# Optimization experiments

Measured on AMD Instinct MI355X. Metric: run time of the kernel, lower is better.

## Reference

```python
import jax, jax.numpy as jnp
import numpy as np
import math

HIDDEN = 512
BATCH, SEQ = 4, 4096


def setup_inputs() -> dict:
    key = jax.random.key(0)
    ks = jax.random.split(key, 7)
    s = 1.0 / math.sqrt(HIDDEN)
    return {
        "X": jax.random.normal(ks[0], (BATCH, SEQ, HIDDEN), dtype=jnp.float32),
        "Wq": jax.random.uniform(ks[1], (HIDDEN, HIDDEN), jnp.float32, -s, s),
        "bq": jax.random.uniform(ks[2], (HIDDEN,), jnp.float32, -s, s),
        "Wk": jax.random.uniform(ks[3], (HIDDEN, HIDDEN), jnp.float32, -s, s),
        "bk": jax.random.uniform(ks[4], (HIDDEN,), jnp.float32, -s, s),
        "Wv": jax.random.uniform(ks[5], (HIDDEN, HIDDEN), jnp.float32, -s, s),
        "bv": jax.random.uniform(ks[6], (HIDDEN,), jnp.float32, -s, s),
    }


def reference(X, Wq, bq, Wk, bk, Wv, bv):
    # Q, K, V projections (torch Linear: y = x @ W.T + b; here W stored as [in, out])
    Q = jnp.einsum("bsd,de->bse", X, Wq) + bq
    K = jnp.einsum("bsd,de->bse", X, Wk) + bk
    V = jnp.einsum("bsd,de->bse", X, Wv) + bv
    scale = 1.0 / math.sqrt(Q.shape[-1])
    scores = jnp.einsum("bqd,bkd->bqk", Q, K) * scale  # [B, S, S]
    weights = jax.nn.softmax(scores, axis=-1)
    return jnp.einsum("bqk,bkd->bqd", weights, V)
```

## Files before the change

kernel.cpp:

```cpp
#include <hip/hip_runtime.h>
#include <hip/hip_bf16.h>
#include <math.h>


typedef __bf16 bfx8 __attribute__((ext_vector_type(8)));
typedef __bf16 bfx4 __attribute__((ext_vector_type(4)));
typedef float  fx4  __attribute__((ext_vector_type(4)));

#define HID   512
#define NBATCH 4
#define SEQ   4096
#define MROWS (NBATCH * SEQ)

constexpr int MODE_BIAS   = 0;
constexpr int MODE_BIAS_T = 1;
constexpr int MODE_EXP    = 2;
constexpr int MODE_DIV    = 3;

__device__ __forceinline__ void gload_lds16(const __bf16* gsrc, __bf16* ldst) {
  __builtin_amdgcn_global_load_lds(
      (const __attribute__((address_space(1))) unsigned int*)gsrc,
      (__attribute__((address_space(3))) unsigned int*)ldst,
      16, 0, 0);
}

__global__ void prep_x_kernel(const float* __restrict__ X, __bf16* __restrict__ Xb) {
  int i = (blockIdx.x * 256 + threadIdx.x) * 4;
  const float4 v = *(const float4*)(X + i);
  bfx4 o;
  o[0] = (__bf16)v.x; o[1] = (__bf16)v.y; o[2] = (__bf16)v.z; o[3] = (__bf16)v.w;
  *(bfx4*)(Xb + i) = o;
}

__global__ void prep_w_kernel(const float* __restrict__ Wq, const float* __restrict__ Wk,
                              const float* __restrict__ Wv, __bf16* __restrict__ Wt) {
  int id  = blockIdx.x * 256 + threadIdx.x;
  int g   = id >> 18;
  int rem = id & ((1 << 18) - 1);
  int i   = rem >> 9;
  int o   = rem & 511;
  const float* W = (g == 0) ? Wq : ((g == 1) ? Wk : Wv);
  Wt[(g << 18) + (o << 9) + i] = (__bf16)W[rem];
}

template <int MODE>
__global__ __launch_bounds__(256)
void gemm_bt(const __bf16* __restrict__ A, const __bf16* __restrict__ B,
             void* __restrict__ Cv, const float* __restrict__ bias,
             float* __restrict__ rowsum,
             int lda, int ldb, int ldc, int K_,
             long sA, long sB, long sC, int sR, float scale) {
  __shared__ __bf16 As[128 * 64];
  __shared__ __bf16 Bs[128 * 64];

  const int z = blockIdx.z;
  A += (long)z * sA;
  B += (long)z * sB;

  const int tid  = threadIdx.x;
  const int lane = tid & 63;
  const int w    = tid >> 6;
  const int wm   = w >> 1, wn = w & 1;
  const int lm   = lane & 15, lq = lane >> 4;

  const int row0 = blockIdx.y * 128;
  const int col0 = blockIdx.x * 128;

  const __bf16* Ag = A + (long)row0 * lda;
  const __bf16* Bg = B + (long)col0 * ldb;

  int srow[4], sgc[4];
#pragma unroll
  for (int it = 0; it < 4; ++it) {
    int s = it * 256 + tid;
    int r = s >> 3, c = s & 7;
    srow[it] = r;
    sgc[it]  = (c ^ (r & 7)) << 3;
  }
  const int ldsbase = (w * 64) * 8;

  fx4 acc[4][4] = {};

  for (int kt = 0; kt < K_; kt += 64) {
    __syncthreads();
#pragma unroll
    for (int it = 0; it < 4; ++it) {
      gload_lds16(Ag + (long)srow[it] * lda + kt + sgc[it], As + it * 2048 + ldsbase);
      gload_lds16(Bg + (long)srow[it] * ldb + kt + sgc[it], Bs + it * 2048 + ldsbase);
    }
    __syncthreads();
#pragma unroll
    for (int kk = 0; kk < 2; ++kk) {
      bfx8 af[4], bfr[4];
#pragma unroll
      for (int t = 0; t < 4; ++t) {
        int ra = wm * 64 + t * 16 + lm;
        int rb = wn * 64 + t * 16 + lm;
        af[t]  = *(const bfx8*)(As + ra * 64 + (((kk * 4 + lq) ^ (ra & 7)) << 3));
        bfr[t] = *(const bfx8*)(Bs + rb * 64 + (((kk * 4 + lq) ^ (rb & 7)) << 3));
      }
#pragma unroll
      for (int mt = 0; mt < 4; ++mt)
#pragma unroll
        for (int nt = 0; nt < 4; ++nt)
          acc[mt][nt] = __builtin_amdgcn_mfma_f32_16x16x32_bf16(af[mt], bfr[nt],
                                                                acc[mt][nt], 0, 0, 0);
    }
  }

  const int gr0 = row0 + wm * 64;
  const int gc0 = col0 + wn * 64;

  if constexpr (MODE == MODE_BIAS || MODE == MODE_BIAS_T) {
    float bvv[4];
#pragma unroll
    for (int nt = 0; nt < 4; ++nt) bvv[nt] = bias[gc0 + nt * 16 + lm];

    if constexpr (MODE == MODE_BIAS) {
      __bf16* C = (__bf16*)Cv;
#pragma unroll
      for (int mt = 0; mt < 4; ++mt)
#pragma unroll
        for (int nt = 0; nt < 4; ++nt)
#pragma unroll
          for (int i = 0; i < 4; ++i) {
            int r = gr0 + mt * 16 + lq * 4 + i;
            int c = gc0 + nt * 16 + lm;
            C[(long)r * ldc + c] = (__bf16)(acc[mt][nt][i] + bvv[nt]);
          }
    } else {
      __bf16* C = (__bf16*)Cv;
#pragma unroll
      for (int mt = 0; mt < 4; ++mt)
#pragma unroll
        for (int nt = 0; nt < 4; ++nt) {
          int c  = gc0 + nt * 16 + lm;
          int rb = gr0 + mt * 16 + lq * 4;
          int b  = rb >> 12;
          int s  = rb & 4095;
          bfx4 pk;
#pragma unroll
          for (int i = 0; i < 4; ++i) pk[i] = (__bf16)(acc[mt][nt][i] + bvv[nt]);
          *(bfx4*)(C + ((long)b * HID + c) * SEQ + s) = pk;
        }
    }
  } else if constexpr (MODE == MODE_EXP) {
    __bf16* C = ((__bf16*)Cv) + (long)z * sC;
    float* rsump = rowsum + (long)z * sR;
#pragma unroll
    for (int mt = 0; mt < 4; ++mt)
#pragma unroll
      for (int i = 0; i < 4; ++i) {
        int r = gr0 + mt * 16 + lq * 4 + i;
        float rs = 0.f;
#pragma unroll
        for (int nt = 0; nt < 4; ++nt) {
          float e = __expf(acc[mt][nt][i] * scale);
          C[(long)r * ldc + gc0 + nt * 16 + lm] = (__bf16)e;
          rs += e;
        }
        rs += __shfl_xor(rs, 1);
        rs += __shfl_xor(rs, 2);
        rs += __shfl_xor(rs, 4);
        rs += __shfl_xor(rs, 8);
        if (lm == 0) atomicAdd(&rsump[r], rs);
      }
  } else {
    float* C = ((float*)Cv) + (long)z * sC;
    const float* rsump = rowsum + (long)z * sR;
#pragma unroll
    for (int mt = 0; mt < 4; ++mt)
#pragma unroll
      for (int i = 0; i < 4; ++i) {
        int r = gr0 + mt * 16 + lq * 4 + i;
        float inv = 1.f / rsump[r];
#pragma unroll
        for (int nt = 0; nt < 4; ++nt)
          C[(long)r * ldc + gc0 + nt * 16 + lm] = acc[mt][nt][i] * inv;
      }
  }
}

extern "C" void kernel_launch(void* const* d_in, const int* in_sizes, int n_in,
                              void* d_out, int out_size, void* d_ws, size_t ws_size,
                              hipStream_t stream) {
  (void)in_sizes; (void)n_in; (void)out_size; (void)ws_size;
  const float* X  = (const float*)d_in[0];
  const float* Wq = (const float*)d_in[1];
  const float* bq = (const float*)d_in[2];
  const float* Wk = (const float*)d_in[3];
  const float* bk = (const float*)d_in[4];
  const float* Wv = (const float*)d_in[5];
  const float* bv = (const float*)d_in[6];
  float* out = (float*)d_out;

  __bf16* Xb     = (__bf16*)d_ws;
  __bf16* Wt     = Xb + (long)MROWS * HID;
  __bf16* Q      = Wt + 3 * HID * HID;
  __bf16* Kb     = Q + (long)MROWS * HID;
  __bf16* Vt     = Kb + (long)MROWS * HID;
  float*  rowsum = (float*)(Vt + (long)MROWS * HID);
  __bf16* E      = (__bf16*)(rowsum + MROWS);

  const float scale = 0.04419417382415922f;

  prep_x_kernel<<<(MROWS * HID) / 1024, 256, 0, stream>>>(X, Xb);
  prep_w_kernel<<<(3 * HID * HID) / 256, 256, 0, stream>>>(Wq, Wk, Wv, Wt);

  gemm_bt<MODE_BIAS><<<dim3(4, 128, 1), 256, 0, stream>>>(
      Xb, Wt, Q, bq, nullptr, HID, HID, HID, HID, 0, 0, 0, 0, 0.f);
  gemm_bt<MODE_BIAS><<<dim3(4, 128, 1), 256, 0, stream>>>(
      Xb, Wt + HID * HID, Kb, bk, nullptr, HID, HID, HID, HID, 0, 0, 0, 0, 0.f);
  gemm_bt<MODE_BIAS_T><<<dim3(4, 128, 1), 256, 0, stream>>>(
      Xb, Wt + 2 * HID * HID, Vt, bv, nullptr, HID, HID, HID, HID, 0, 0, 0, 0, 0.f);

  (void)hipMemsetAsync(rowsum, 0, MROWS * sizeof(float), stream);

  gemm_bt<MODE_EXP><<<dim3(32, 32, NBATCH), 256, 0, stream>>>(
      Q, Kb, E, nullptr, rowsum, HID, HID, SEQ, HID,
      (long)SEQ * HID, (long)SEQ * HID, (long)SEQ * SEQ, SEQ, scale);

  gemm_bt<MODE_DIV><<<dim3(4, 32, NBATCH), 256, 0, stream>>>(
      E, Vt, out, nullptr, rowsum, SEQ, SEQ, HID, SEQ,
      (long)SEQ * SEQ, (long)HID * SEQ, (long)SEQ * HID, SEQ, 0.f);
}
```

Before: 352.4 us.

## Fuse QKV projections, fold softmax scale into Q, split-K the PV GEMM

Merges the three projection GEMMs into one launch that routes output tiles to Q, K or transposed V by column group. The softmax scale, and log2(e) when the exp2 builtin is available, is pre-multiplied into Q so the exp epilogue uses a bare exp2. The attention-times-V GEMM is split into two K halves, which doubles the block count, and accumulates into an output that is zeroed first using float atomics. This trades extra memset and atomic traffic for better GPU occupancy and fewer launches. It also changes bf16 rounding of Q.

```diff
diff --git a/kernel.cpp b/kernel.cpp
--- a/kernel.cpp
+++ b/kernel.cpp
@@ -12,10 +12,17 @@
 #define SEQ   4096
 #define MROWS (NBATCH * SEQ)
 
-constexpr int MODE_BIAS   = 0;
-constexpr int MODE_BIAS_T = 1;
-constexpr int MODE_EXP    = 2;
-constexpr int MODE_DIV    = 3;
+#if __has_builtin(__builtin_amdgcn_exp2f)
+#define EXPFN(x) __builtin_amdgcn_exp2f(x)
+#define QSCALE 0.06375871589f
+#else
+#define EXPFN(x) __expf(x)
+#define QSCALE 0.04419417382f
+#endif
+
+constexpr int MODE_QKV = 0;
+constexpr int MODE_EXP = 2;
+constexpr int MODE_DIV = 3;
 
 __device__ __forceinline__ void gload_lds16(const __bf16* gsrc, __bf16* ldst) {
   __builtin_amdgcn_global_load_lds(
@@ -46,16 +53,20 @@
 template <int MODE>
 __global__ __launch_bounds__(256)
 void gemm_bt(const __bf16* __restrict__ A, const __bf16* __restrict__ B,
-             void* __restrict__ Cv, const float* __restrict__ bias,
-             float* __restrict__ rowsum,
+             void* __restrict__ C0v, void* __restrict__ C1v, void* __restrict__ C2v,
+             const float* __restrict__ b0, const float* __restrict__ b1,
+             const float* __restrict__ b2, float* __restrict__ rowsum,
              int lda, int ldb, int ldc, int K_,
-             long sA, long sB, long sC, int sR, float scale) {
+             long sA, long sB, long sC, int sR) {
   __shared__ __bf16 As[128 * 64];
   __shared__ __bf16 Bs[128 * 64];
 
   const int z = blockIdx.z;
-  A += (long)z * sA;
-  B += (long)z * sB;
+  int zb, koff;
+  if constexpr (MODE == MODE_DIV) { zb = z >> 1; koff = (z & 1) * 2048; }
+  else                            { zb = z;      koff = 0; }
+  A += (long)zb * sA + koff;
+  B += (long)zb * sB + koff;
 
   const int tid  = threadIdx.x;
   const int lane = tid & 63;
@@ -111,13 +122,16 @@
   const int gr0 = row0 + wm * 64;
   const int gc0 = col0 + wn * 64;
 
-  if constexpr (MODE == MODE_BIAS || MODE == MODE_BIAS_T) {
+  if constexpr (MODE == MODE_QKV) {
+    const int g   = col0 >> 9;
+    const int lc0 = (col0 & 511) + wn * 64;
+    const float* bias = (g == 0) ? b0 : ((g == 1) ? b1 : b2);
     float bvv[4];
 #pragma unroll
-    for (int nt = 0; nt < 4; ++nt) bvv[nt] = bias[gc0 + nt * 16 + lm];
-
-    if constexpr (MODE == MODE_BIAS) {
-      __bf16* C = (__bf16*)Cv;
+    for (int nt = 0; nt < 4; ++nt) bvv[nt] = bias[lc0 + nt * 16 + lm];
+
+    if (g == 0) {
+      __bf16* C = (__bf16*)C0v;
 #pragma unroll
       for (int mt = 0; mt < 4; ++mt)
 #pragma unroll
@@ -125,16 +139,27 @@
 #pragma unroll
           for (int i = 0; i < 4; ++i) {
             int r = gr0 + mt * 16 + lq * 4 + i;
-            int c = gc0 + nt * 16 + lm;
-            C[(long)r * ldc + c] = (__bf16)(acc[mt][nt][i] + bvv[nt]);
+            C[(long)r * HID + lc0 + nt * 16 + lm] =
+                (__bf16)((acc[mt][nt][i] + bvv[nt]) * QSCALE);
+          }
+    } else if (g == 1) {
+      __bf16* C = (__bf16*)C1v;
+#pragma unroll
+      for (int mt = 0; mt < 4; ++mt)
+#pragma unroll
+        for (int nt = 0; nt < 4; ++nt)
+#pragma unroll
+          for (int i = 0; i < 4; ++i) {
+            int r = gr0 + mt * 16 + lq * 4 + i;
+            C[(long)r * HID + lc0 + nt * 16 + lm] = (__bf16)(acc[mt][nt][i] + bvv[nt]);
           }
     } else {
-      __bf16* C = (__bf16*)Cv;
+      __bf16* C = (__bf16*)C2v;
 #pragma unroll
       for (int mt = 0; mt < 4; ++mt)
 #pragma unroll
         for (int nt = 0; nt < 4; ++nt) {
-          int c  = gc0 + nt * 16 + lm;
+          int c  = lc0 + nt * 16 + lm;
           int rb = gr0 + mt * 16 + lq * 4;
           int b  = rb >> 12;
           int s  = rb & 4095;
@@ -145,7 +170,7 @@
         }
     }
   } else if constexpr (MODE == MODE_EXP) {
-    __bf16* C = ((__bf16*)Cv) + (long)z * sC;
+    __bf16* C = ((__bf16*)C0v) + (long)z * sC;
     float* rsump = rowsum + (long)z * sR;
 #pragma unroll
     for (int mt = 0; mt < 4; ++mt)
@@ -155,7 +180,7 @@
         float rs = 0.f;
 #pragma unroll
         for (int nt = 0; nt < 4; ++nt) {
-          float e = __expf(acc[mt][nt][i] * scale);
+          float e = EXPFN(acc[mt][nt][i]);
           C[(long)r * ldc + gc0 + nt * 16 + lm] = (__bf16)e;
           rs += e;
         }
@@ -166,8 +191,8 @@
         if (lm == 0) atomicAdd(&rsump[r], rs);
       }
   } else {
-    float* C = ((float*)Cv) + (long)z * sC;
-    const float* rsump = rowsum + (long)z * sR;
+    float* C = ((float*)C0v) + (long)zb * sC;
+    const float* rsump = rowsum + (long)zb * sR;
 #pragma unroll
     for (int mt = 0; mt < 4; ++mt)
 #pragma unroll
@@ -176,7 +201,7 @@
         float inv = 1.f / rsump[r];
 #pragma unroll
         for (int nt = 0; nt < 4; ++nt)
-          C[(long)r * ldc + gc0 + nt * 16 + lm] = acc[mt][nt][i] * inv;
+          atomicAdd(&C[(long)r * ldc + gc0 + nt * 16 + lm], acc[mt][nt][i] * inv);
       }
   }
 }
@@ -202,25 +227,21 @@
   float*  rowsum = (float*)(Vt + (long)MROWS * HID);
   __bf16* E      = (__bf16*)(rowsum + MROWS);
 
-  const float scale = 0.04419417382415922f;
-
   prep_x_kernel<<<(MROWS * HID) / 1024, 256, 0, stream>>>(X, Xb);
   prep_w_kernel<<<(3 * HID * HID) / 256, 256, 0, stream>>>(Wq, Wk, Wv, Wt);
 
-  gemm_bt<MODE_BIAS><<<dim3(4, 128, 1), 256, 0, stream>>>(
-      Xb, Wt, Q, bq, nullptr, HID, HID, HID, HID, 0, 0, 0, 0, 0.f);
-  gemm_bt<MODE_BIAS><<<dim3(4, 128, 1), 256, 0, stream>>>(
-      Xb, Wt + HID * HID, Kb, bk, nullptr, HID, HID, HID, HID, 0, 0, 0, 0, 0.f);
-  gemm_bt<MODE_BIAS_T><<<dim3(4, 128, 1), 256, 0, stream>>>(
-      Xb, Wt + 2 * HID * HID, Vt, bv, nullptr, HID, HID, HID, HID, 0, 0, 0, 0, 0.f);
-
   (void)hipMemsetAsync(rowsum, 0, MROWS * sizeof(float), stream);
+  (void)hipMemsetAsync(out, 0, (long)MROWS * HID * sizeof(float), stream);
+
+  gemm_bt<MODE_QKV><<<dim3(12, 128, 1), 256, 0, stream>>>(
+      Xb, Wt, Q, Kb, Vt, bq, bk, bv, nullptr,
+      HID, HID, HID, HID, 0, 0, 0, 0);
 
   gemm_bt<MODE_EXP><<<dim3(32, 32, NBATCH), 256, 0, stream>>>(
-      Q, Kb, E, nullptr, rowsum, HID, HID, SEQ, HID,
-      (long)SEQ * HID, (long)SEQ * HID, (long)SEQ * SEQ, SEQ, scale);
-
-  gemm_bt<MODE_DIV><<<dim3(4, 32, NBATCH), 256, 0, stream>>>(
-      E, Vt, out, nullptr, rowsum, SEQ, SEQ, HID, SEQ,
-      (long)SEQ * SEQ, (long)HID * SEQ, (long)SEQ * HID, SEQ, 0.f);
-}
+      Q, Kb, E, nullptr, nullptr, nullptr, nullptr, nullptr, rowsum,
+      HID, HID, SEQ, HID, (long)SEQ * HID, (long)SEQ * HID, (long)SEQ * SEQ, SEQ);
+
+  gemm_bt<MODE_DIV><<<dim3(4, 32, NBATCH * 2), 256, 0, stream>>>(
+      E, Vt, out, nullptr, nullptr, nullptr, nullptr, nullptr, rowsum,
+      SEQ, SEQ, HID, 2048, (long)SEQ * SEQ, (long)HID * SEQ, (long)SEQ * HID, SEQ);
+}
```

After: 364.4 us. 1.03x slower.
